# Performance work log

Measured on AMD Instinct MI355X. Metric: run time of the kernel, lower is better.

Reference implementation:

```python
import jax, jax.numpy as jnp
import numpy as np
import math

N_HEAD = 16

def setup_inputs() -> dict:
    key = jax.random.key(0)
    k1, k2, k3, k4, k5 = jax.random.split(key, 5)
    B, S, D = 2, 2048, 1024
    return {
        "hidden_states": jax.random.normal(k1, (B, S, D), dtype=jnp.float32),
        "c_attn_w": jax.random.normal(k2, (D, 3 * D), dtype=jnp.float32) * 0.02,
        "c_attn_b": jax.random.normal(k3, (3 * D,), dtype=jnp.float32) * 0.02,
        "c_proj_w": jax.random.normal(k4, (D, D), dtype=jnp.float32) * 0.02,
        "c_proj_b": jax.random.normal(k5, (D,), dtype=jnp.float32) * 0.02,
    }

def reference(hidden_states, c_attn_w, c_attn_b, c_proj_w, c_proj_b):
    B, S, D = hidden_states.shape
    H = N_HEAD
    hd = D // H
    # GPT-2 Conv1D: x @ W + b, W is [in, out]
    qkv = hidden_states @ c_attn_w + c_attn_b            # [B,S,3D]
    q, k, v = jnp.split(qkv, 3, axis=-1)                 # each [B,S,D]
    # sparsify_q/k/v_fn are identity hooks in this config
    def to_heads(x):
        return x.reshape(B, S, H, hd).transpose(0, 2, 1, 3)  # [B,H,S,hd]
    q, k, v = to_heads(q), to_heads(k), to_heads(v)
    scores = jnp.einsum("bhqd,bhkd->bhqk", q, k) / math.sqrt(hd)  # [B,H,S,S]
    causal = jnp.triu(jnp.ones((S, S), dtype=bool), k=1)
    scores = jnp.where(causal, jnp.finfo(scores.dtype).min, scores)
    attn = jax.nn.softmax(scores, axis=-1)
    out = jnp.einsum("bhqk,bhkd->bhqd", attn, v)         # [B,H,S,hd]
    out = out.transpose(0, 2, 1, 3).reshape(B, S, D)
    return out @ c_proj_w + c_proj_b
```

## Files before the change

### kernel.cpp

```cpp
#include <hip/hip_runtime.h>
#include <stdint.h>


#define B_   2
#define S_   2048
#define D_   1024
#define H_   16
#define HD_  64

typedef __bf16 bf16x8 __attribute__((ext_vector_type(8)));
typedef float  f32x4  __attribute__((ext_vector_type(4)));
typedef uint32_t u32x4 __attribute__((ext_vector_type(4)));

__device__ __forceinline__ float b2f(uint16_t u) {
    union { uint32_t i; float f; } x; x.i = ((uint32_t)u) << 16; return x.f;
}
__device__ __forceinline__ uint16_t f2b(float f) {
    uint32_t x = __builtin_bit_cast(uint32_t, f);
    x += 0x7fffu + ((x >> 16) & 1u);
    return (uint16_t)(x >> 16);
}
__device__ __forceinline__ float sq(float f) {
    return fminf(fmaxf(f, -1e4f), 1e4f);
}
__device__ __forceinline__ void async16(const void* g, void* l) {
    __builtin_amdgcn_global_load_lds(
        (const __attribute__((address_space(1))) void*)g,
        (__attribute__((address_space(3))) void*)l, 16, 0, 0);
}

__global__ __launch_bounds__(64)
void kcode(uint16_t* out, float v) { if (threadIdx.x == 0) out[0] = f2b(v); }

__global__ __launch_bounds__(256)
void kconvert(const float* __restrict__ in, uint16_t* __restrict__ out, int n) {
    int i = (blockIdx.x * 256 + threadIdx.x) * 4;
    if (i >= n) return;
    float4 v = *(const float4*)(in + i);
    ushort4 o;
    o.x = f2b(v.x); o.y = f2b(v.y); o.z = f2b(v.z); o.w = f2b(v.w);
    *(ushort4*)(out + i) = o;
}

__global__ __launch_bounds__(256)
void kconvert_bias(const float* __restrict__ ab, const float* __restrict__ pb,
                   uint16_t* __restrict__ bA, uint16_t* __restrict__ bP) {
    int i = (blockIdx.x * 256 + threadIdx.x) * 4;
    const float* src = (i < 3072) ? ab + i : pb + (i - 3072);
    uint16_t*   dst = (i < 3072) ? bA + i : bP + (i - 3072);
    float4 v = *(const float4*)src;
    ushort4 o;
    o.x = f2b(v.x); o.y = f2b(v.y); o.z = f2b(v.z); o.w = f2b(v.w);
    *(ushort4*)dst = o;
}

__global__ __launch_bounds__(256)
void ktranspose_cvt(const float* __restrict__ in, uint16_t* __restrict__ out,
                    int rows, int cols) {
    __shared__ __attribute__((aligned(16))) uint16_t tile[64][68];
    const int tid = threadIdx.x, tx = tid & 15, ty = tid >> 4;
    const int c0 = blockIdx.x * 64, r0 = blockIdx.y * 64;
#pragma unroll
    for (int p = 0; p < 4; ++p) {
        int rr = ty + p * 16;
        float4 v = *(const float4*)(in + (size_t)(r0 + rr) * cols + c0 + tx * 4);
        tile[rr][tx * 4 + 0] = f2b(v.x);
        tile[rr][tx * 4 + 1] = f2b(v.y);
        tile[rr][tx * 4 + 2] = f2b(v.z);
        tile[rr][tx * 4 + 3] = f2b(v.w);
    }
    __syncthreads();
#pragma unroll
    for (int p = 0; p < 4; ++p) {
        int rr = ty + p * 16;
        ushort4 v;
        v.x = tile[tx * 4 + 0][rr];
        v.y = tile[tx * 4 + 1][rr];
        v.z = tile[tx * 4 + 2][rr];
        v.w = tile[tx * 4 + 3][rr];
        *(ushort4*)(out + (size_t)(c0 + rr) * rows + r0 + tx * 4) = v;
    }
}

__global__ __launch_bounds__(256, 2)
void kgemm_qkv(const uint16_t* __restrict__ A, const uint16_t* __restrict__ Bt,
               const uint16_t* __restrict__ bias,
               uint16_t* __restrict__ Qb, uint16_t* __restrict__ Kb,
               uint16_t* __restrict__ Vt) {
    constexpr int KD = 1024;
    __shared__ __attribute__((aligned(16))) uint16_t smem[2 * 128 * 32];
    uint16_t* As = smem;
    uint16_t* Bs = smem + 128 * 32;
    const int tid = threadIdx.x, lane = tid & 63, wid = tid >> 6;
    const int r = lane & 15, qd = lane >> 4;
    const int bm = blockIdx.x * 128, bn = blockIdx.y * 128;
    const int wm = (wid & 1) * 64, wn = (wid >> 1) * 64;
    const int sel = (int)blockIdx.y >> 3;
    f32x4 acc[4][4] = {};

    auto stage = [&](int k0) {
#pragma unroll
        for (int half = 0; half < 2; ++half) {
            int s = half * 256 + tid;
            int row = s >> 2;
            int kq = (s & 3) ^ (row & 3);
            async16(A  + (size_t)(bm + row) * KD + k0 + kq * 8, As + s * 8);
            async16(Bt + (size_t)(bn + row) * KD + k0 + kq * 8, Bs + s * 8);
        }
    };

    if (sel != 2) {
        for (int k0 = 0; k0 < KD; k0 += 32) {
            stage(k0);
            __syncthreads();
            bf16x8 af[4], bfr[4];
#pragma unroll
            for (int i = 0; i < 4; ++i) {
                int ra = wm + i * 16 + r;
                af[i]  = *(const bf16x8*)(As + ((ra * 4) + (qd ^ (ra & 3))) * 8);
                int rb = wn + i * 16 + r;
                bfr[i] = *(const bf16x8*)(Bs + ((rb * 4) + (qd ^ (rb & 3))) * 8);
            }
#pragma unroll
            for (int i = 0; i < 4; ++i)
#pragma unroll
                for (int j = 0; j < 4; ++j)
                    acc[i][j] = __builtin_amdgcn_mfma_f32_16x16x32_bf16(
                        bfr[j], af[i], acc[i][j], 0, 0, 0);
            __syncthreads();
        }
        const float SCq = 0.1803368801111204f;
        uint16_t* dst = sel ? Kb : Qb;
#pragma unroll
        for (int j = 0; j < 4; ++j) {
            int n0 = bn + wn + j * 16 + qd * 4;
            ushort4 b4 = *(const ushort4*)(bias + n0);
            float bv0 = b2f(b4.x), bv1 = b2f(b4.y),
                  bv2 = b2f(b4.z), bv3 = b2f(b4.w);
            int d = n0 & 1023, h = d >> 6, e0 = d & 63;
#pragma unroll
            for (int i = 0; i < 4; ++i) {
                int m = bm + wm + i * 16 + r;
                int bb = m >> 11, s = m & 2047;
                float v0 = acc[i][j][0] + bv0, v1 = acc[i][j][1] + bv1,
                      v2 = acc[i][j][2] + bv2, v3 = acc[i][j][3] + bv3;
                if (sel == 0) { v0 *= SCq; v1 *= SCq; v2 *= SCq; v3 *= SCq; }
                ushort4 o;
                o.x = f2b(sq(v0)); o.y = f2b(sq(v1));
                o.z = f2b(sq(v2)); o.w = f2b(sq(v3));
                *(ushort4*)(dst + (((size_t)bb * H_ + h) * S_ + s) * HD_ + e0) = o;
            }
        }
    } else {
        for (int k0 = 0; k0 < KD; k0 += 32) {
            stage(k0);
            __syncthreads();
            bf16x8 af[4], bfr[4];
#pragma unroll
            for (int i = 0; i < 4; ++i) {
                int ra = wm + i * 16 + r;
                af[i]  = *(const bf16x8*)(As + ((ra * 4) + (qd ^ (ra & 3))) * 8);
                int rb = wn + i * 16 + r;
                bfr[i] = *(const bf16x8*)(Bs + ((rb * 4) + (qd ^ (rb & 3))) * 8);
            }
#pragma unroll
            for (int i = 0; i < 4; ++i)
#pragma unroll
                for (int j = 0; j < 4; ++j)
                    acc[i][j] = __builtin_amdgcn_mfma_f32_16x16x32_bf16(
                        af[i], bfr[j], acc[i][j], 0, 0, 0);
            __syncthreads();
        }
#pragma unroll
        for (int j = 0; j < 4; ++j) {
            int n = bn + wn + j * 16 + r;
            float bv = b2f(bias[n]);
            int d = n & 1023, h = d >> 6, e = d & 63;
#pragma unroll
            for (int i = 0; i < 4; ++i) {
                int m0 = bm + wm + i * 16 + qd * 4;
                int bb = m0 >> 11, s0 = m0 & 2047;
                ushort4 o;
                o.x = f2b(sq(acc[i][j][0] + bv));
                o.y = f2b(sq(acc[i][j][1] + bv));
                o.z = f2b(sq(acc[i][j][2] + bv));
                o.w = f2b(sq(acc[i][j][3] + bv));
                *(ushort4*)(Vt + (((size_t)bb * H_ + h) * HD_ + e) * S_ + s0) = o;
            }
        }
    }
}

__global__ __launch_bounds__(256, 2)
void kgemm_proj(const uint16_t* __restrict__ A, const uint16_t* __restrict__ Bt,
                const uint16_t* __restrict__ bias, float* __restrict__ out) {
    constexpr int KD = 1024;
    __shared__ __attribute__((aligned(16))) uint16_t smem[(64 + 128) * 32];
    uint16_t* As = smem;
    uint16_t* Bs = smem + 64 * 32;
    const int tid = threadIdx.x, lane = tid & 63, wid = tid >> 6;
    const int r = lane & 15, qd = lane >> 4;
    const int bm = blockIdx.x * 64, bn = blockIdx.y * 128;
    const int wm = (wid & 1) * 32, wn = (wid >> 1) * 64;
    f32x4 acc[2][4] = {};

    for (int k0 = 0; k0 < KD; k0 += 32) {
        {
            int s = tid;
            int row = s >> 2;
            int kq = (s & 3) ^ (row & 3);
            async16(A + (size_t)(bm + row) * KD + k0 + kq * 8, As + s * 8);
        }
#pragma unroll
        for (int half = 0; half < 2; ++half) {
            int s = half * 256 + tid;
            int row = s >> 2;
            int kq = (s & 3) ^ (row & 3);
            async16(Bt + (size_t)(bn + row) * KD + k0 + kq * 8, Bs + s * 8);
        }
        __syncthreads();
        bf16x8 af[2], bfr[4];
#pragma unroll
        for (int i = 0; i < 2; ++i) {
            int ra = wm + i * 16 + r;
            af[i] = *(const bf16x8*)(As + ((ra * 4) + (qd ^ (ra & 3))) * 8);
        }
#pragma unroll
        for (int j = 0; j < 4; ++j) {
            int rb = wn + j * 16 + r;
            bfr[j] = *(const bf16x8*)(Bs + ((rb * 4) + (qd ^ (rb & 3))) * 8);
        }
#pragma unroll
        for (int i = 0; i < 2; ++i)
#pragma unroll
            for (int j = 0; j < 4; ++j)
                acc[i][j] = __builtin_amdgcn_mfma_f32_16x16x32_bf16(
                    bfr[j], af[i], acc[i][j], 0, 0, 0);
        __syncthreads();
    }

#pragma unroll
    for (int i = 0; i < 2; ++i) {
        int m = bm + wm + i * 16 + r;
#pragma unroll
        for (int j = 0; j < 4; ++j) {
            int n0 = bn + wn + j * 16 + qd * 4;
            ushort4 b4 = *(const ushort4*)(bias + n0);
            float4 o;
            o.x = sq(acc[i][j][0] + b2f(b4.x));
            o.y = sq(acc[i][j][1] + b2f(b4.y));
            o.z = sq(acc[i][j][2] + b2f(b4.z));
            o.w = sq(acc[i][j][3] + b2f(b4.w));
            *(float4*)(out + (size_t)m * 1024 + n0) = o;
        }
    }
}

__global__ __launch_bounds__(256, 4)
void kattn(const uint16_t* __restrict__ Q, const uint16_t* __restrict__ K,
           const uint16_t* __restrict__ Vt, uint16_t* __restrict__ O) {
    const int d_  = (int)blockIdx.y * 32 + (int)blockIdx.x;
    const int bh  = (d_ & 7) + 8 * ((d_ >> 3) & 3);
    const int qt  = 31 - (d_ >> 5);
    const int tid = threadIdx.x, lane = tid & 63, wid = tid >> 6;
    const int r = lane & 15, qd = lane >> 4;
    const uint16_t* Qb = Q  + (size_t)bh * S_ * HD_;
    const uint16_t* Kb = K  + (size_t)bh * S_ * HD_;
    const uint16_t* Vb = Vt + (size_t)bh * HD_ * S_;
    const int b = bh >> 4, h = bh & 15;

    __shared__ __attribute__((aligned(16))) uint16_t Ks[2][64 * 64];
    __shared__ __attribute__((aligned(16))) uint16_t Vs[2][64 * 64];

    const int T = qt + 1;

    auto stage = [&](int t) {
        const int k0 = t * 64;
        uint16_t* Kd = Ks[t & 1];
        uint16_t* Vd = Vs[t & 1];
#pragma unroll
        for (int i = 0; i < 2; ++i) {
            int s = i * 256 + tid;
            int row = s >> 3, c = (s & 7) ^ (row & 7);
            async16(Kb + (size_t)(k0 + row) * HD_ + c * 8, Kd + s * 8);
        }
#pragma unroll
        for (int i = 0; i < 2; ++i) {
            int s = i * 256 + tid;
            int row = s >> 3, c = (s & 7) ^ (row & 7);
            async16(Vb + (size_t)row * S_ + k0 + c * 8, Vd + s * 8);
        }
    };

    stage(0);

    const int q0 = qt * 64;
    const int qrow = q0 + wid * 16 + r;
    const bf16x8 qf0 = *(const bf16x8*)(Qb + (size_t)qrow * HD_ + qd * 8);
    const bf16x8 qf1 = *(const bf16x8*)(Qb + (size_t)qrow * HD_ + 32 + qd * 8);

    const int kswz0 = (qd ^ (r & 7)) * 8;
    const int kswz1 = ((4 + qd) ^ (r & 7)) * 8;

    f32x4 oacc[4] = {};
    float lsum = 0.f;

#pragma unroll 1
    for (int t = 0; t < T; ++t) {
        __syncthreads();
        if (t + 1 < T) stage(t + 1);

        const uint16_t* Kc = Ks[t & 1];
        const uint16_t* Vc = Vs[t & 1];

        f32x4 sacc[4] = {};
        __builtin_amdgcn_s_setprio(1);
#pragma unroll
        for (int n = 0; n < 4; ++n) {
            int row = n * 16 + r;
            bf16x8 kf0 = *(const bf16x8*)(Kc + row * 64 + kswz0);
            bf16x8 kf1 = *(const bf16x8*)(Kc + row * 64 + kswz1);
            sacc[n] = __builtin_amdgcn_mfma_f32_16x16x32_bf16(kf0, qf0, sacc[n], 0, 0, 0);
            sacc[n] = __builtin_amdgcn_mfma_f32_16x16x32_bf16(kf1, qf1, sacc[n], 0, 0, 0);
        }
        __builtin_amdgcn_s_setprio(0);
        if (t == T - 1) {
#pragma unroll
            for (int n = 0; n < 4; ++n) {
                int kvb = t * 64 + n * 16 + qd * 4;
#pragma unroll
                for (int g = 0; g < 4; ++g)
                    if (kvb + g > qrow) sacc[n][g] = -3e38f;
            }
        }
        uint32_t D0[4], D1[4];
#pragma unroll
        for (int n = 0; n < 4; ++n) {
            float p0 = exp2f(fminf(sacc[n][0], 20.f));
            float p1 = exp2f(fminf(sacc[n][1], 20.f));
            float p2 = exp2f(fminf(sacc[n][2], 20.f));
            float p3 = exp2f(fminf(sacc[n][3], 20.f));
            lsum += (p0 + p1) + (p2 + p3);
            asm("v_cvt_pk_bf16_f32 %0, %1, %2" : "=v"(D0[n]) : "v"(p0), "v"(p1));
            asm("v_cvt_pk_bf16_f32 %0, %1, %2" : "=v"(D1[n]) : "v"(p2), "v"(p3));
        }
#pragma unroll
        for (int m = 0; m < 2; ++m) {
            asm("v_permlane32_swap_b32 %0, %1"
                : "+v"(D0[2 * m]), "+v"(D0[2 * m + 1]));
            asm("v_permlane32_swap_b32 %0, %1"
                : "+v"(D1[2 * m]), "+v"(D1[2 * m + 1]));
            asm("v_permlane16_swap_b32 %0, %1"
                : "+v"(D0[2 * m]), "+v"(D0[2 * m + 1]));
            asm("v_permlane16_swap_b32 %0, %1"
                : "+v"(D1[2 * m]), "+v"(D1[2 * m + 1]));
        }
        __builtin_amdgcn_s_setprio(1);
#pragma unroll
        for (int ks = 0; ks < 2; ++ks) {
            u32x4 w;
            w[0] = D0[2 * ks]; w[1] = D1[2 * ks];
            w[2] = D0[2 * ks + 1]; w[3] = D1[2 * ks + 1];
            bf16x8 pf = __builtin_bit_cast(bf16x8, w);
            int c = ((ks * 4 + qd) ^ (r & 7)) * 8;
#pragma unroll
            for (int j = 0; j < 4; ++j) {
                bf16x8 vf = *(const bf16x8*)(Vc + (j * 16 + r) * 64 + c);
                oacc[j] = __builtin_amdgcn_mfma_f32_16x16x32_bf16(pf, vf, oacc[j], 0, 0, 0);
            }
        }
        __builtin_amdgcn_s_setprio(0);
    }

    float ls = lsum;
    ls += __shfl_xor(ls, 16);
    ls += __shfl_xor(ls, 32);
#pragma unroll
    for (int g = 0; g < 4; ++g) {
        float inv = 1.0f / __shfl(ls, qd * 4 + g);
        int rowg = q0 + wid * 16 + qd * 4 + g;
        size_t base = ((size_t)b * S_ + rowg) * D_ + h * HD_;
#pragma unroll
        for (int j = 0; j < 4; ++j)
            O[base + j * 16 + r] = f2b(sq(oacc[j][g] * inv));
    }
}

extern "C" void kernel_launch(void* const* d_in, const int* in_sizes, int n_in,
                              void* d_out, int out_size, void* d_ws, size_t ws_size,
                              hipStream_t stream) {
    uint16_t* ws = (uint16_t*)d_ws;

    const int exp_sizes[5] = {4194304, 3145728, 3072, 1048576, 1024};
    if (n_in != 5) { kcode<<<1, 64, 0, stream>>>((uint16_t*)d_out, 2950.f); return; }
    for (int i = 0; i < 5; ++i)
        if (in_sizes[i] != exp_sizes[i]) {
            kcode<<<1, 64, 0, stream>>>((uint16_t*)d_out, 3000.f + 100.f * i); return;
        }
    if (out_size != 4194304) { kcode<<<1, 64, 0, stream>>>((uint16_t*)d_out, 2900.f); return; }

    uint16_t* WtA = ws;
    uint16_t* WtP = WtA + 3145728;
    uint16_t* bA  = WtP + 1048576;
    uint16_t* bP  = bA  + 4096;
    uint16_t* Qb  = bP  + 4096;
    uint16_t* Kb  = Qb  + 4194304;
    uint16_t* Vt  = Kb  + 4194304;
    uint16_t* HO  = Vt  + 4194304;
    const size_t NEED = (size_t)((HO + 4194304) - ws) * 2 + 16;
    if (ws_size < NEED) {
        kcode<<<1, 64, 0, stream>>>((uint16_t*)d_out, 1000.f + (float)(ws_size >> 20));
        return;
    }

    kconvert<<<4096, 256, 0, stream>>>((const float*)d_in[0], HO, 4194304);
    kconvert_bias<<<4, 256, 0, stream>>>((const float*)d_in[2], (const float*)d_in[4],
                                         bA, bP);
    ktranspose_cvt<<<dim3(48, 16), 256, 0, stream>>>((const float*)d_in[1], WtA, 1024, 3072);
    ktranspose_cvt<<<dim3(16, 16), 256, 0, stream>>>((const float*)d_in[3], WtP, 1024, 1024);

    kgemm_qkv<<<dim3(32, 24), 256, 0, stream>>>(HO, WtA, bA, Qb, Kb, Vt);
    kattn<<<dim3(32, 32), 256, 0, stream>>>(Qb, Kb, Vt, HO);
    kgemm_proj<<<dim3(64, 8), 256, 0, stream>>>(HO, WtP, bP, (float*)d_out);
}
```

Measured before the change: 185.3 us.

## Double-buffer GEMM smem tiles and load V fragments directly from global in attention

```diff
diff --git a/kernel.cpp b/kernel.cpp
--- a/kernel.cpp
+++ b/kernel.cpp
@@ -88,9 +88,7 @@
                uint16_t* __restrict__ Qb, uint16_t* __restrict__ Kb,
                uint16_t* __restrict__ Vt) {
     constexpr int KD = 1024;
-    __shared__ __attribute__((aligned(16))) uint16_t smem[2 * 128 * 32];
-    uint16_t* As = smem;
-    uint16_t* Bs = smem + 128 * 32;
+    __shared__ __attribute__((aligned(16))) uint16_t smem[2][8192];
     const int tid = threadIdx.x, lane = tid & 63, wid = tid >> 6;
     const int r = lane & 15, qd = lane >> 4;
     const int bm = blockIdx.x * 128, bn = blockIdx.y * 128;
@@ -98,7 +96,9 @@
     const int sel = (int)blockIdx.y >> 3;
     f32x4 acc[4][4] = {};
 
-    auto stage = [&](int k0) {
+    auto stage = [&](int k0, int buf) {
+        uint16_t* As = smem[buf];
+        uint16_t* Bs = smem[buf] + 4096;
 #pragma unroll
         for (int half = 0; half < 2; ++half) {
             int s = half * 256 + tid;
@@ -109,10 +109,14 @@
         }
     };
 
+    stage(0, 0);
+
     if (sel != 2) {
-        for (int k0 = 0; k0 < KD; k0 += 32) {
-            stage(k0);
+        for (int t = 0; t < 32; ++t) {
             __syncthreads();
+            if (t + 1 < 32) stage((t + 1) * 32, (t + 1) & 1);
+            const uint16_t* As = smem[t & 1];
+            const uint16_t* Bs = smem[t & 1] + 4096;
             bf16x8 af[4], bfr[4];
 #pragma unroll
             for (int i = 0; i < 4; ++i) {
@@ -127,7 +131,6 @@
                 for (int j = 0; j < 4; ++j)
                     acc[i][j] = __builtin_amdgcn_mfma_f32_16x16x32_bf16(
                         bfr[j], af[i], acc[i][j], 0, 0, 0);
-            __syncthreads();
         }
         const float SCq = 0.1803368801111204f;
         uint16_t* dst = sel ? Kb : Qb;
@@ -152,9 +155,11 @@
             }
         }
     } else {
-        for (int k0 = 0; k0 < KD; k0 += 32) {
-            stage(k0);
+        for (int t = 0; t < 32; ++t) {
             __syncthreads();
+            if (t + 1 < 32) stage((t + 1) * 32, (t + 1) & 1);
+            const uint16_t* As = smem[t & 1];
+            const uint16_t* Bs = smem[t & 1] + 4096;
             bf16x8 af[4], bfr[4];
 #pragma unroll
             for (int i = 0; i < 4; ++i) {
@@ -169,7 +174,6 @@
                 for (int j = 0; j < 4; ++j)
                     acc[i][j] = __builtin_amdgcn_mfma_f32_16x16x32_bf16(
                         af[i], bfr[j], acc[i][j], 0, 0, 0);
-            __syncthreads();
         }
 #pragma unroll
         for (int j = 0; j < 4; ++j) {
@@ -195,16 +199,16 @@
 void kgemm_proj(const uint16_t* __restrict__ A, const uint16_t* __restrict__ Bt,
                 const uint16_t* __restrict__ bias, float* __restrict__ out) {
     constexpr int KD = 1024;
-    __shared__ __attribute__((aligned(16))) uint16_t smem[(64 + 128) * 32];
-    uint16_t* As = smem;
-    uint16_t* Bs = smem + 64 * 32;
+    __shared__ __attribute__((aligned(16))) uint16_t smem[2][6144];
     const int tid = threadIdx.x, lane = tid & 63, wid = tid >> 6;
     const int r = lane & 15, qd = lane >> 4;
     const int bm = blockIdx.x * 64, bn = blockIdx.y * 128;
     const int wm = (wid & 1) * 32, wn = (wid >> 1) * 64;
     f32x4 acc[2][4] = {};
 
-    for (int k0 = 0; k0 < KD; k0 += 32) {
+    auto stage = [&](int k0, int buf) {
+        uint16_t* As = smem[buf];
+        uint16_t* Bs = smem[buf] + 2048;
         {
             int s = tid;
             int row = s >> 2;
@@ -218,7 +222,15 @@
             int kq = (s & 3) ^ (row & 3);
             async16(Bt + (size_t)(bn + row) * KD + k0 + kq * 8, Bs + s * 8);
         }
+    };
+
+    stage(0, 0);
+
+    for (int t = 0; t < 32; ++t) {
         __syncthreads();
+        if (t + 1 < 32) stage((t + 1) * 32, (t + 1) & 1);
+        const uint16_t* As = smem[t & 1];
+        const uint16_t* Bs = smem[t & 1] + 2048;
         bf16x8 af[2], bfr[4];
 #pragma unroll
         for (int i = 0; i < 2; ++i) {
@@ -236,7 +248,6 @@
             for (int j = 0; j < 4; ++j)
                 acc[i][j] = __builtin_amdgcn_mfma_f32_16x16x32_bf16(
                     bfr[j], af[i], acc[i][j], 0, 0, 0);
-        __syncthreads();
     }
 
 #pragma unroll
@@ -270,29 +281,21 @@
     const int b = bh >> 4, h = bh & 15;
 
     __shared__ __attribute__((aligned(16))) uint16_t Ks[2][64 * 64];
-    __shared__ __attribute__((aligned(16))) uint16_t Vs[2][64 * 64];
 
     const int T = qt + 1;
 
-    auto stage = [&](int t) {
+    auto stageK = [&](int t) {
         const int k0 = t * 64;
         uint16_t* Kd = Ks[t & 1];
-        uint16_t* Vd = Vs[t & 1];
 #pragma unroll
         for (int i = 0; i < 2; ++i) {
             int s = i * 256 + tid;
             int row = s >> 3, c = (s & 7) ^ (row & 7);
             async16(Kb + (size_t)(k0 + row) * HD_ + c * 8, Kd + s * 8);
         }
-#pragma unroll
-        for (int i = 0; i < 2; ++i) {
-            int s = i * 256 + tid;
-            int row = s >> 3, c = (s & 7) ^ (row & 7);
-            async16(Vb + (size_t)row * S_ + k0 + c * 8, Vd + s * 8);
-        }
     };
 
-    stage(0);
+    stageK(0);
 
     const int q0 = qt * 64;
     const int qrow = q0 + wid * 16 + r;
@@ -301,17 +304,27 @@
 
     const int kswz0 = (qd ^ (r & 7)) * 8;
     const int kswz1 = ((4 + qd) ^ (r & 7)) * 8;
+    const uint16_t* Vl = Vb + (size_t)r * S_ + qd * 8;
 
     f32x4 oacc[4] = {};
     float lsum = 0.f;
 
 #pragma unroll 1
     for (int t = 0; t < T; ++t) {
+        const int k0 = t * 64;
         __syncthreads();
-        if (t + 1 < T) stage(t + 1);
+
+        bf16x8 vfr[2][4];
+#pragma unroll
+        for (int ks = 0; ks < 2; ++ks)
+#pragma unroll
+            for (int j = 0; j < 4; ++j)
+                vfr[ks][j] = *(const bf16x8*)(Vl + (size_t)(j * 16) * S_ +
+                                              k0 + ks * 32);
+
+        if (t + 1 < T) stageK(t + 1);
 
         const uint16_t* Kc = Ks[t & 1];
-        const uint16_t* Vc = Vs[t & 1];
 
         f32x4 sacc[4] = {};
         __builtin_amdgcn_s_setprio(1);
@@ -327,7 +340,7 @@
         if (t == T - 1) {
 #pragma unroll
             for (int n = 0; n < 4; ++n) {
-                int kvb = t * 64 + n * 16 + qd * 4;
+                int kvb = k0 + n * 16 + qd * 4;
 #pragma unroll
                 for (int g = 0; g < 4; ++g)
                     if (kvb + g > qrow) sacc[n][g] = -3e38f;
@@ -362,12 +375,10 @@
             w[0] = D0[2 * ks]; w[1] = D1[2 * ks];
             w[2] = D0[2 * ks + 1]; w[3] = D1[2 * ks + 1];
             bf16x8 pf = __builtin_bit_cast(bf16x8, w);
-            int c = ((ks * 4 + qd) ^ (r & 7)) * 8;
-#pragma unroll
-            for (int j = 0; j < 4; ++j) {
-                bf16x8 vf = *(const bf16x8*)(Vc + (j * 16 + r) * 64 + c);
-                oacc[j] = __builtin_amdgcn_mfma_f32_16x16x32_bf16(pf, vf, oacc[j], 0, 0, 0);
-            }
+#pragma unroll
+            for (int j = 0; j < 4; ++j)
+                oacc[j] = __builtin_amdgcn_mfma_f32_16x16x32_bf16(
+                    pf, vfr[ks][j], oacc[j], 0, 0, 0);
         }
         __builtin_amdgcn_s_setprio(0);
     }
```

After: 217.3 us. +17.3%, slower.
